# Optimization experiments

Measured on AMD Instinct MI355X. Metric: run time of the kernel, lower is better.

Reference implementation:

```python
import jax, jax.numpy as jnp
import numpy as np


def setup_inputs() -> dict:
    B, S, D, V = 2, 4096, 512, 32000
    FE_START, FE_LEN = 5, 3062          # user-controllable span [5, 3067)
    ADV_START, ADV_LEN = 1000, 64       # adversarial suffix block
    ML = ADV_START - FE_START           # 995 = max_left_shift
    MR = FE_LEN - (ADV_START - FE_START + ADV_LEN)  # 2003 = max_right_shift
    key = jax.random.key(0)
    k1, k2 = jax.random.split(key)
    input_ids = jax.random.randint(k1, (B, S), 0, V, dtype=jnp.int32)
    suffix_mask = jnp.zeros((B, S), dtype=bool).at[:, ADV_START:ADV_START + ADV_LEN].set(True)
    # param initialized like _create_parameters: delta at index max_left_shift
    param = jnp.zeros((1, ML + MR + 1), dtype=jnp.float32).at[0, ML].set(1.0)
    emb_weight = jax.random.normal(k2, (V, D), dtype=jnp.float32) * 0.02
    return {
        'input_ids': input_ids, 'suffix_mask': suffix_mask,
        'param': param, 'emb_weight': emb_weight,
        'fe_start': FE_START, 'fe_len': FE_LEN, 'adv_len': ADV_LEN,
        'max_left_shift': ML, 'max_right_shift': MR,
    }


def _padded_kernel(param, ml, mr):
    left_pad = max(0, mr - ml)
    right_pad = max(0, ml - mr)
    # F.pad then flip, as in torch forward
    return jnp.flip(jnp.pad(param, ((0, 0), (left_pad, right_pad)))[0])  # (Kp,)


def reference(input_ids, suffix_mask, param, emb_weight,
              fe_start, fe_len, adv_len, max_left_shift, max_right_shift):
    B, S = input_ids.shape
    D = emb_weight.shape[1]
    Kp = 2 * max(max_left_shift, max_right_shift) + 1
    p = Kp // 2  # 'same' padding
    pk = _padded_kernel(param, max_left_shift, max_right_shift).astype(emb_weight.dtype)

    embeds = emb_weight[input_ids]                       # (B,S,D)
    fe = embeds[:, fe_start:fe_start + fe_len]           # frontend-user gather (contiguous)
    fe_pad = jnp.pad(fe, ((0, 0), (p, p), (0, 0)))       # (B, F+2p, D)
    # depthwise conv1d with a single shared kernel == Toeplitz matmul
    off = jnp.arange(fe_len + 2 * p)[None, :] - jnp.arange(fe_len)[:, None]
    W = jnp.where((off >= 0) & (off < Kp), pk[jnp.clip(off, 0, Kp - 1)], 0.0)  # (F, F+2p)
    new_fe = jnp.einsum('tu,bud->btd', W, fe_pad)        # (B,F,D)
    # scatter-concat: other[:extra0] | shifted user span | other[extra1:]
    out_embeds = jnp.concatenate(
        [embeds[:, :fe_start], new_fe, embeds[:, fe_start + fe_len:]], axis=1)

    # ----- id path (no_grad in original) -----
    L = adv_len
    ms = p - jnp.argmax(pk == 1.0)                       # mask_shift
    a0 = jnp.argmax(suffix_mask, axis=-1)                # (B,) current_start
    ns = a0 + ms                                         # new_start
    idx = jnp.arange(S - L)[None, :]
    src = idx + L * (idx >= a0[:, None])                 # skip the adv block
    nonadv = jnp.take_along_axis(input_ids, src, axis=1)             # (B,S-L)
    adv = jnp.take_along_axis(input_ids, a0[:, None] + jnp.arange(L)[None, :], axis=1)
    j = jnp.arange(S)[None, :]
    in_adv = (j >= ns[:, None]) & (j < ns[:, None] + L)
    idx_non = jnp.clip(jnp.where(j < ns[:, None], j, j - L), 0, S - L - 1)
    idx_adv = jnp.clip(j - ns[:, None], 0, L - 1)
    out_ids = jnp.where(in_adv,
                        jnp.take_along_axis(adv, idx_adv, axis=1),
                        jnp.take_along_axis(nonadv, idx_non, axis=1))
    return out_embeds, out_ids
```

## Files before the change

kernel.cpp:

```cpp
#include <hip/hip_runtime.h>
#include <limits.h>

#define BB 2
#define SS 4096
#define DD 512
#define FE_START 5
#define FE_LEN 3062
#define ADV_LEN 64
#define ML 995
#define MR 2003
#define KP (2 * MR + 1)
#define PHALF (KP / 2)
#define PARAM_LEN (ML + MR + 1)


#define RPB 8
#define NT 256
#define TAP_CAP 512

__global__ __launch_bounds__(NT) void ABS_fused(
        const int* __restrict__ ids,
        const unsigned char* __restrict__ mask_bytes,
        const float* __restrict__ param,
        const float* __restrict__ emb,
        float* __restrict__ out) {
    __shared__ int   s_tapo[TAP_CAP];
    __shared__ float s_tapw[TAP_CAP];
    __shared__ int s_nnz, s_jmax, s_a0b, s_a0i, s_layout;

    const int tid = threadIdx.x;
    const int block_row = blockIdx.x * RPB;
    const int b = block_row / SS;

    if (tid == 0) { s_nnz = 0; s_jmax = -1; s_a0b = INT_MAX; s_a0i = INT_MAX; }
    __syncthreads();

    for (int j = tid; j < PARAM_LEN; j += NT) {
        float w = param[j];
        if (w != 0.0f) {
            int slot = atomicAdd(&s_nnz, 1);
            if (slot < TAP_CAP) { s_tapo[slot] = 995 - j; s_tapw[slot] = w; }
        }
        if (w == 1.0f) atomicMax(&s_jmax, j);
    }

    const unsigned long long* m8 = (const unsigned long long*)mask_bytes;
    for (int u = b * (SS / 8) + tid, e = (b + 1) * (SS / 8); u < e; u += NT) {
        unsigned long long w = m8[u];
        if (w) {
            int fb = 8 * u + (__ffsll((long long)w) - 1) / 8 - b * SS;
            atomicMin(&s_a0b, fb);
        }
    }
    __syncthreads();

    if (tid == 0) {
        int f = s_a0b;
        int layout = 4;
        if (f != INT_MAX)
            layout = (f + 1 < SS && mask_bytes[b * SS + f + 1] != 0) ? 1 : 4;
        s_layout = layout;
    }
    __syncthreads();

    if (s_layout == 4) {
        for (int u = b * (SS / 2) + tid, e = (b + 1) * (SS / 2); u < e; u += NT) {
            unsigned long long w = m8[u];
            if (w) {
                int base = 2 * u - b * SS;
                if ((unsigned int)w)         atomicMin(&s_a0i, base);
                if ((unsigned int)(w >> 32)) atomicMin(&s_a0i, base + 1);
            }
        }
        __syncthreads();
    }

    const int  nnz      = (s_nnz < TAP_CAP) ? s_nnz : TAP_CAP;
    const bool overflow = (s_nnz > TAP_CAP);
    const int  a0r      = (s_layout == 1) ? s_a0b : s_a0i;
    const int  a0       = (a0r == INT_MAX) ? 0 : a0r;
    const int  ms       = (s_jmax >= 0) ? (s_jmax - 995) : PHALF;

    const int d4   = tid & 127;
    const int half = tid >> 7;
    for (int it = 0; it < RPB / 2; ++it) {
        const int bt = block_row + it * 2 + half;
        const int t  = bt - b * SS;
        float4* out4 = (float4*)(out + (size_t)bt * DD);
        if (t < FE_START || t >= FE_START + FE_LEN) {
            const int id = ids[bt];
            out4[d4] = ((const float4*)(emb + (size_t)id * DD))[d4];
        } else {
            const int tt = t - FE_START;
            float4 acc = make_float4(0.f, 0.f, 0.f, 0.f);
            if (!overflow) {
                for (int k = 0; k < nnz; ++k) {
                    const int s = tt + s_tapo[k];
                    const float w = s_tapw[k];
                    if (s >= 0 && s < FE_LEN) {
                        const int id = ids[b * SS + FE_START + s];
                        const float4 v = ((const float4*)(emb + (size_t)id * DD))[d4];
                        acc.x += w * v.x; acc.y += w * v.y;
                        acc.z += w * v.z; acc.w += w * v.w;
                    }
                }
            } else {
                for (int j = 0; j < PARAM_LEN; ++j) {
                    const float w = param[j];
                    if (w != 0.0f) {
                        const int s = tt + 995 - j;
                        if (s >= 0 && s < FE_LEN) {
                            const int id = ids[b * SS + FE_START + s];
                            const float4 v = ((const float4*)(emb + (size_t)id * DD))[d4];
                            acc.x += w * v.x; acc.y += w * v.y;
                            acc.z += w * v.z; acc.w += w * v.w;
                        }
                    }
                }
            }
            out4[d4] = acc;
        }
    }

    if (tid < RPB) {
        const int bt = block_row + tid;
        const int j  = bt - b * SS;
        const int ns = a0 + ms;
        int outid;
        if (j >= ns && j < ns + ADV_LEN) {
            outid = ids[b * SS + a0 + (j - ns)];
        } else {
            int k = (j < ns) ? j : (j - ADV_LEN);
            k = min(max(k, 0), SS - ADV_LEN - 1);
            outid = ids[b * SS + k + ((k >= a0) ? ADV_LEN : 0)];
        }
        out[(size_t)BB * SS * DD + bt] = (float)outid;
    }
}

extern "C" void kernel_launch(void* const* d_in, const int* in_sizes, int n_in,
                              void* d_out, int out_size, void* d_ws, size_t ws_size,
                              hipStream_t stream) {
    const int* ids = (const int*)d_in[0];
    const unsigned char* mask = (const unsigned char*)d_in[1];
    const float* param = (const float*)d_in[2];
    const float* emb = (const float*)d_in[3];
    float* out = (float*)d_out;

    ABS_fused<<<(BB * SS) / RPB, NT, 0, stream>>>(ids, mask, param, emb, out);
}
```

Baseline: 125.0 us.

## Vectorize param scan, merge layout detection, double rows per block, use nontemporal stores

Reads the param vector as float4 chunks, merges the mask layout check into the first-byte scan so one barrier and one serial step disappear, and doubles rows per block so the per-block setup cost is spread over more output rows. The output stores become nontemporal, and the id path now runs before the embedding loop. Each block still rescans the whole param and mask, and with half as many blocks the GPU may have less parallelism to hide latency.

```diff
diff --git a/kernel.cpp b/kernel.cpp
--- a/kernel.cpp
+++ b/kernel.cpp
@@ -9,14 +9,15 @@
 #define ADV_LEN 64
 #define ML 995
 #define MR 2003
-#define KP (2 * MR + 1)
-#define PHALF (KP / 2)
+#define PHALF 2003
 #define PARAM_LEN (ML + MR + 1)
 
 
-#define RPB 8
+#define RPB 16
 #define NT 256
 #define TAP_CAP 512
+
+typedef float vfloat4 __attribute__((ext_vector_type(4)));
 
 __global__ __launch_bounds__(NT) void ABS_fused(
         const int* __restrict__ ids,
@@ -26,48 +27,54 @@
         float* __restrict__ out) {
     __shared__ int   s_tapo[TAP_CAP];
     __shared__ float s_tapw[TAP_CAP];
-    __shared__ int s_nnz, s_jmax, s_a0b, s_a0i, s_layout;
+    __shared__ int s_nnz, s_jmax, s_a0pack, s_a0i;
 
     const int tid = threadIdx.x;
     const int block_row = blockIdx.x * RPB;
     const int b = block_row / SS;
 
-    if (tid == 0) { s_nnz = 0; s_jmax = -1; s_a0b = INT_MAX; s_a0i = INT_MAX; }
+    if (tid == 0) { s_nnz = 0; s_jmax = -1; s_a0pack = INT_MAX; s_a0i = INT_MAX; }
     __syncthreads();
 
-    for (int j = tid; j < PARAM_LEN; j += NT) {
-        float w = param[j];
-        if (w != 0.0f) {
-            int slot = atomicAdd(&s_nnz, 1);
-            if (slot < TAP_CAP) { s_tapo[slot] = 995 - j; s_tapw[slot] = w; }
+    const vfloat4* p4 = (const vfloat4*)param;
+    for (int q = tid; q < 750; q += NT) {
+        float w[4];
+        if (q < 749) { vfloat4 v = p4[q]; w[0]=v.x; w[1]=v.y; w[2]=v.z; w[3]=v.w; }
+        else { w[0]=param[2996]; w[1]=param[2997]; w[2]=param[2998]; w[3]=0.f; }
+        #pragma unroll
+        for (int c = 0; c < 4; ++c) {
+            const int j = 4 * q + c;
+            const float wc = w[c];
+            if (wc != 0.0f) {
+                int slot = atomicAdd(&s_nnz, 1);
+                if (slot < TAP_CAP) { s_tapo[slot] = 995 - j; s_tapw[slot] = wc; }
+                if (wc == 1.0f) atomicMax(&s_jmax, j);
+            }
         }
-        if (w == 1.0f) atomicMax(&s_jmax, j);
     }
 
     const unsigned long long* m8 = (const unsigned long long*)mask_bytes;
     for (int u = b * (SS / 8) + tid, e = (b + 1) * (SS / 8); u < e; u += NT) {
         unsigned long long w = m8[u];
         if (w) {
-            int fb = 8 * u + (__ffsll((long long)w) - 1) / 8 - b * SS;
-            atomicMin(&s_a0b, fb);
+            const int k = (__ffsll((long long)w) - 1) >> 3;
+            const int fb = (u * 8 + k) - b * SS;
+            unsigned int nb;
+            if (k < 7)            nb = (unsigned int)((w >> (8 * (k + 1))) & 0xffull);
+            else if (fb + 1 < SS) nb = mask_bytes[b * SS + fb + 1];
+            else                  nb = 0;
+            atomicMin(&s_a0pack, fb * 2 + (nb ? 0 : 1));
         }
     }
     __syncthreads();
 
-    if (tid == 0) {
-        int f = s_a0b;
-        int layout = 4;
-        if (f != INT_MAX)
-            layout = (f + 1 < SS && mask_bytes[b * SS + f + 1] != 0) ? 1 : 4;
-        s_layout = layout;
-    }
-    __syncthreads();
-
-    if (s_layout == 4) {
+    const int pack = s_a0pack;
+    const bool layout_int = (pack == INT_MAX) || (pack & 1);
+    if (layout_int) {
         for (int u = b * (SS / 2) + tid, e = (b + 1) * (SS / 2); u < e; u += NT) {
             unsigned long long w = m8[u];
             if (w) {
-                int base = 2 * u - b * SS;
+                const int base = 2 * u - b * SS;
                 if ((unsigned int)w)         atomicMin(&s_a0i, base);
                 if ((unsigned int)(w >> 32)) atomicMin(&s_a0i, base + 1);
             }
@@ -77,50 +84,10 @@
 
     const int  nnz      = (s_nnz < TAP_CAP) ? s_nnz : TAP_CAP;
     const bool overflow = (s_nnz > TAP_CAP);
-    const int  a0r      = (s_layout == 1) ? s_a0b : s_a0i;
-    const int  a0       = (a0r == INT_MAX) ? 0 : a0r;
-    const int  ms       = (s_jmax >= 0) ? (s_jmax - 995) : PHALF;
-
-    const int d4   = tid & 127;
-    const int half = tid >> 7;
-    for (int it = 0; it < RPB / 2; ++it) {
-        const int bt = block_row + it * 2 + half;
-        const int t  = bt - b * SS;
-        float4* out4 = (float4*)(out + (size_t)bt * DD);
-        if (t < FE_START || t >= FE_START + FE_LEN) {
-            const int id = ids[bt];
-            out4[d4] = ((const float4*)(emb + (size_t)id * DD))[d4];
-        } else {
-            const int tt = t - FE_START;
-            float4 acc = make_float4(0.f, 0.f, 0.f, 0.f);
-            if (!overflow) {
-                for (int k = 0; k < nnz; ++k) {
-                    const int s = tt + s_tapo[k];
-                    const float w = s_tapw[k];
-                    if (s >= 0 && s < FE_LEN) {
-                        const int id = ids[b * SS + FE_START + s];
-                        const float4 v = ((const float4*)(emb + (size_t)id * DD))[d4];
-                        acc.x += w * v.x; acc.y += w * v.y;
-                        acc.z += w * v.z; acc.w += w * v.w;
-                    }
-                }
-            } else {
-                for (int j = 0; j < PARAM_LEN; ++j) {
-                    const float w = param[j];
-                    if (w != 0.0f) {
-                        const int s = tt + 995 - j;
-                        if (s >= 0 && s < FE_LEN) {
-                            const int id = ids[b * SS + FE_START + s];
-                            const float4 v = ((const float4*)(emb + (size_t)id * DD))[d4];
-                            acc.x += w * v.x; acc.y += w * v.y;
-                            acc.z += w * v.z; acc.w += w * v.w;
-                        }
-                    }
-                }
-            }
-            out4[d4] = acc;
-        }
-    }
+    int a0;
+    if (layout_int) a0 = (s_a0i == INT_MAX) ? 0 : s_a0i;
+    else            a0 = pack >> 1;
+    const int ms = (s_jmax >= 0) ? (s_jmax - 995) : PHALF;
 
     if (tid < RPB) {
         const int bt = block_row + tid;
@@ -134,7 +101,48 @@
             k = min(max(k, 0), SS - ADV_LEN - 1);
             outid = ids[b * SS + k + ((k >= a0) ? ADV_LEN : 0)];
         }
-        out[(size_t)BB * SS * DD + bt] = (float)outid;
+        __builtin_nontemporal_store((float)outid,
+                                    out + (size_t)BB * SS * DD + bt);
+    }
+
+    const int d4   = tid & 127;
+    const int half = tid >> 7;
+    for (int it = 0; it < RPB / 2; ++it) {
+        const int bt = block_row + it * 2 + half;
+        const int t  = bt - b * SS;
+        vfloat4* outp = (vfloat4*)(out + (size_t)bt * DD) + d4;
+        if (t < FE_START || t >= FE_START + FE_LEN) {
+            const int id = ids[bt];
+            const vfloat4 v = ((const vfloat4*)(emb + (size_t)id * DD))[d4];
+            __builtin_nontemporal_store(v, outp);
+        } else {
+            const int tt = t - FE_START;
+            vfloat4 acc = (vfloat4){0.f, 0.f, 0.f, 0.f};
+            if (!overflow) {
+                for (int k = 0; k < nnz; ++k) {
+                    const int s = tt + s_tapo[k];
+                    const float w = s_tapw[k];
+                    if (s >= 0 && s < FE_LEN) {
+                        const int id = ids[b * SS + FE_START + s];
+                        const vfloat4 v = ((const vfloat4*)(emb + (size_t)id * DD))[d4];
+                        acc += w * v;
+                    }
+                }
+            } else {
+                for (int j = 0; j < PARAM_LEN; ++j) {
+                    const float w = param[j];
+                    if (w != 0.0f) {
+                        const int s = tt + 995 - j;
+                        if (s >= 0 && s < FE_LEN) {
+                            const int id = ids[b * SS + FE_START + s];
+                            const vfloat4 v = ((const vfloat4*)(emb + (size_t)id * DD))[d4];
+                            acc += w * v;
+                        }
+                    }
+                }
+            }
+            __builtin_nontemporal_store(acc, outp);
+        }
     }
 }
 
```

Result: no change. 123.9 us (-0.9%).
